# Kernel optimization log

Measured on AMD Instinct MI355X. Metric: run time of the kernel, lower is better.

Reference implementation:

```python
import jax, jax.numpy as jnp
import numpy as np

N_USER, N_FOOD, N_ING, N_CAT, N_HAB = 50000, 50000, 50000, 5000, 5000
N_NODES = N_USER + N_FOOD + N_ING + N_CAT + N_HAB  # 160000
E = 600000
R = 8
D = 128  # common_dim == hidden_dim


def _linear(x, W, b):
    # W: (in, out)
    return x @ W + b


def _rgcn_conv(x, src, dst, edge_type, W, root, bias):
    """PyG RGCNConv with aggr='mean': out = x@root + bias + sum_r mean_{r-edges into i}(W_r x_j)."""
    n = x.shape[0]
    out = x @ root + bias
    for r in range(R):  # static small loop over relations
        mask = (edge_type == r)
        h_r = x @ W[r]                          # (N, O)
        msg = h_r[src] * mask[:, None].astype(x.dtype)  # (E, O)
        s = jax.ops.segment_sum(msg, dst, num_segments=n)
        cnt = jax.ops.segment_sum(mask.astype(x.dtype), dst, num_segments=n)
        out = out + s / jnp.maximum(cnt, 1.0)[:, None]
    return out


def setup_inputs() -> dict:
    key = jax.random.key(0)
    ks = jax.random.split(key, 32)
    s = 0.05
    inp = {
        'x_user': jax.random.normal(ks[0], (N_USER, 256), jnp.float32),
        'x_food': jax.random.normal(ks[1], (N_FOOD, 128), jnp.float32),
        'x_ingredient': jax.random.normal(ks[2], (N_ING, 128), jnp.float32),
        'x_category': jax.random.normal(ks[3], (N_CAT, 64), jnp.float32),
        'x_habit': jax.random.normal(ks[4], (N_HAB, 64), jnp.float32),
        'edge_index': jax.random.randint(ks[5], (2, E), 0, N_NODES, jnp.int32),
        'edge_type': jax.random.randint(ks[6], (E,), 0, R, jnp.int32),
        # init linears (in, out)
        'Wu': jax.random.normal(ks[7], (256, D), jnp.float32) * s,
        'bu': jnp.zeros((D,), jnp.float32),
        'Wf': jax.random.normal(ks[8], (128, D), jnp.float32) * s,
        'bf': jnp.zeros((D,), jnp.float32),
        'Wi': jax.random.normal(ks[9], (128, D), jnp.float32) * s,
        'bi': jnp.zeros((D,), jnp.float32),
        'Wc': jax.random.normal(ks[10], (64, D), jnp.float32) * s,
        'bc': jnp.zeros((D,), jnp.float32),
        'Wh': jax.random.normal(ks[11], (64, D), jnp.float32) * s,
        'bh': jnp.zeros((D,), jnp.float32),
        # conv1
        'W1': jax.random.normal(ks[12], (R, D, D), jnp.float32) * s,
        'root1': jax.random.normal(ks[13], (D, D), jnp.float32) * s,
        'bias1': jnp.zeros((D,), jnp.float32),
        # conv2
        'W2': jax.random.normal(ks[14], (R, D, D), jnp.float32) * s,
        'root2': jax.random.normal(ks[15], (D, D), jnp.float32) * s,
        'bias2': jnp.zeros((D,), jnp.float32),
    }
    return inp


def reference(x_user, x_food, x_ingredient, x_category, x_habit,
              edge_index, edge_type,
              Wu, bu, Wf, bf, Wi, bi, Wc, bc, Wh, bh,
              W1, root1, bias1, W2, root2, bias2):
    # per-type input projections then concat in fixed order
    x_all = jnp.concatenate([
        _linear(x_user, Wu, bu),
        _linear(x_food, Wf, bf),
        _linear(x_ingredient, Wi, bi),
        _linear(x_category, Wc, bc),
        _linear(x_habit, Wh, bh),
    ], axis=0)  # (N_NODES, D)
    src, dst = edge_index[0], edge_index[1]
    x = _rgcn_conv(x_all, src, dst, edge_type, W1, root1, bias1)
    x = jax.nn.relu(x)
    # dropout is identity in eval mode
    x = _rgcn_conv(x, src, dst, edge_type, W2, root2, bias2)
    return x
```

## Files before the change

kernel.cpp:

```cpp
#include <hip/hip_runtime.h>

typedef unsigned short ushort_t;
typedef unsigned int uint_t;
typedef __attribute__((ext_vector_type(8))) __bf16 bf16x8;
typedef __attribute__((ext_vector_type(4))) float f32x4;
typedef __attribute__((ext_vector_type(4))) uint_t uint4v;

#define NN 160000
#define DD 128
#define EE 600000
#define RR 8
#define NRR (NN * RR)
#define WTOT 376832

__device__ __forceinline__ ushort_t f2b(float f) {
  uint_t u = __float_as_uint(f);
  u = u + 0x7fffu + ((u >> 16) & 1u);
  return (ushort_t)(u >> 16);
}
__device__ __forceinline__ float b2f(ushort_t u) {
  return __uint_as_float(((uint_t)u) << 16);
}

struct WSrcs { const float* s[9]; };

__global__ void wconv_all_kernel(WSrcs srcs, ushort_t* __restrict__ wbuf) {
  int i = blockIdx.x * blockDim.x + threadIdx.x;
  if (i >= WTOT) return;
  int m, start, K;
  if      (i < 32768)  { m = 0; start = 0;      K = 256; }
  else if (i < 49152)  { m = 1; start = 32768;  K = 128; }
  else if (i < 65536)  { m = 2; start = 49152;  K = 128; }
  else if (i < 73728)  { m = 3; start = 65536;  K = 64;  }
  else if (i < 81920)  { m = 4; start = 73728;  K = 64;  }
  else if (i < 98304)  { m = 5; start = 81920;  K = 128; }
  else if (i < 114688) { m = 6; start = 98304;  K = 128; }
  else if (i < 245760) { m = 7; start = 114688; K = 128; }
  else                 { m = 8; start = 245760; K = 128; }
  int local = i - start;
  int per = K * 128;
  int mat = local / per, rem = local - mat * per;
  int k = rem >> 7, n = rem & 127;
  wbuf[start + mat * per + n * K + k] = f2b(srcs.s[m][local]);
}

__global__ __launch_bounds__(256, 2) void gemm_proj(
    const float* __restrict__ Ain, const ushort_t* __restrict__ WT,
    const float* __restrict__ bias, ushort_t* __restrict__ Cout, int M, int K) {
  __shared__ ushort_t As[128 * 128];
  __shared__ ushort_t Ws[128 * 128];
  const int tid = threadIdx.x;
  const int bm = blockIdx.x * 128;
  const int wave = tid >> 6, lane = tid & 63;
  const int lr = lane & 15;
  const int lg = lane >> 4;

  f32x4 acc[2][8];
#pragma unroll
  for (int mt = 0; mt < 2; ++mt)
#pragma unroll
    for (int nt = 0; nt < 8; ++nt) acc[mt][nt] = {0.f, 0.f, 0.f, 0.f};

  for (int k0 = 0; k0 < K; k0 += 128) {
#pragma unroll
    for (int it = 0; it < 8; ++it) {
      int row = it * 16 + (tid >> 4);
      int c = tid & 15;
      uint4v val = {0, 0, 0, 0};
      int grow = bm + row, gk = k0 + c * 8;
      if (grow < M && gk < K) {
        const float* ap = Ain + (size_t)grow * K + gk;
        float4 v0 = *(const float4*)ap;
        float4 v1 = *(const float4*)(ap + 4);
        val[0] = (uint_t)f2b(v0.x) | ((uint_t)f2b(v0.y) << 16);
        val[1] = (uint_t)f2b(v0.z) | ((uint_t)f2b(v0.w) << 16);
        val[2] = (uint_t)f2b(v1.x) | ((uint_t)f2b(v1.y) << 16);
        val[3] = (uint_t)f2b(v1.z) | ((uint_t)f2b(v1.w) << 16);
      }
      *(uint4v*)&As[row * 128 + ((c ^ (row & 7)) * 8)] = val;
    }
#pragma unroll
    for (int it = 0; it < 8; ++it) {
      int n = it * 16 + (tid >> 4);
      int c = tid & 15;
      uint4v val = {0, 0, 0, 0};
      int gk = k0 + c * 8;
      if (gk < K)
        val = *(const uint4v*)(WT + (size_t)n * K + gk);
      *(uint4v*)&Ws[n * 128 + ((c ^ (n & 7)) * 8)] = val;
    }
    __syncthreads();
#pragma unroll
    for (int ks = 0; ks < 4; ++ks) {
      int chunk = ks * 4 + lg;
      bf16x8 af[2], bfr[8];
#pragma unroll
      for (int mt = 0; mt < 2; ++mt) {
        int row = wave * 32 + mt * 16 + lr;
        af[mt] = *(const bf16x8*)&As[row * 128 + ((chunk ^ (row & 7)) * 8)];
      }
#pragma unroll
      for (int nt = 0; nt < 8; ++nt) {
        int n = nt * 16 + lr;
        bfr[nt] = *(const bf16x8*)&Ws[n * 128 + ((chunk ^ (n & 7)) * 8)];
      }
#pragma unroll
      for (int mt = 0; mt < 2; ++mt)
#pragma unroll
        for (int nt = 0; nt < 8; ++nt)
          acc[mt][nt] = __builtin_amdgcn_mfma_f32_16x16x32_bf16(
              af[mt], bfr[nt], acc[mt][nt], 0, 0, 0);
    }
    __syncthreads();
  }

  float bv[8];
#pragma unroll
  for (int nt = 0; nt < 8; ++nt) bv[nt] = bias[nt * 16 + lr];

#pragma unroll
  for (int mt = 0; mt < 2; ++mt) {
    int rbase = bm + wave * 32 + mt * 16 + lg * 4;
#pragma unroll
    for (int i = 0; i < 4; ++i) {
      int row = rbase + i;
      if (row >= M) continue;
#pragma unroll
      for (int nt = 0; nt < 8; ++nt)
        Cout[(size_t)row * 128 + nt * 16 + lr] = f2b(acc[mt][nt][i] + bv[nt]);
    }
  }
}

template <bool RELU_BF>
__global__ __launch_bounds__(256, 3) void rgcn_conv(
    const ushort_t* __restrict__ xin, const int* __restrict__ seg_off,
    const int* __restrict__ sorted_src,
    const ushort_t* __restrict__ WrT,
    const ushort_t* __restrict__ rootT,
    const float* __restrict__ bias,
    float* __restrict__ fout, ushort_t* __restrict__ bfout) {
  __shared__ ushort_t As[64 * 128];
  __shared__ ushort_t Ws[128 * 128];
  const int tid = threadIdx.x;
  const int bm = blockIdx.x * 64;
  const int wave = tid >> 6, lane = tid & 63;
  const int lr = lane & 15, lg = lane >> 4;
  const int grp = tid >> 4;
  const int sl = tid & 15;

  f32x4 acc[8];
#pragma unroll
  for (int nt = 0; nt < 8; ++nt) acc[nt] = {0.f, 0.f, 0.f, 0.f};

  for (int ph = 0; ph < 9; ++ph) {
    if (ph == 0) {
#pragma unroll
      for (int q = 0; q < 4; ++q) {
        int row = q * 16 + grp;
        uint4v val = *(const uint4v*)(xin + (size_t)(bm + row) * DD + sl * 8);
        *(uint4v*)&As[row * 128 + ((sl ^ (row & 7)) * 8)] = val;
      }
    } else {
      const int rel = ph - 1;
      int gs[4], ge[4];
#pragma unroll
      for (int q = 0; q < 4; ++q) {
        const int* sp = seg_off + (size_t)rel * NN + (bm + q * 16 + grp);
        gs[q] = sp[0];
        ge[q] = sp[1];
      }
      int fs[4];
#pragma unroll
      for (int q = 0; q < 4; ++q)
        fs[q] = (ge[q] > gs[q]) ? sorted_src[gs[q]] : 0;
      uint4v fv[4];
#pragma unroll
      for (int q = 0; q < 4; ++q)
        fv[q] = *(const uint4v*)(xin + (size_t)fs[q] * DD + sl * 8);

#pragma unroll
      for (int q = 0; q < 4; ++q) {
        int row = q * 16 + grp;
        int cnt = ge[q] - gs[q];
        uint4v o = {0, 0, 0, 0};
        if (cnt == 1) {
          o = fv[q];
        } else if (cnt > 1) {
          float a[8];
#pragma unroll
          for (int j = 0; j < 4; ++j) {
            a[j * 2]     = b2f((ushort_t)(fv[q][j] & 0xffff));
            a[j * 2 + 1] = b2f((ushort_t)(fv[q][j] >> 16));
          }
          for (int i = gs[q] + 1; i < ge[q]; ++i) {
            int s = sorted_src[i];
            uint4v v2 = *(const uint4v*)(xin + (size_t)s * DD + sl * 8);
#pragma unroll
            for (int j = 0; j < 4; ++j) {
              a[j * 2]     += b2f((ushort_t)(v2[j] & 0xffff));
              a[j * 2 + 1] += b2f((ushort_t)(v2[j] >> 16));
            }
          }
          float sc = 1.0f / (float)cnt;
#pragma unroll
          for (int j = 0; j < 4; ++j)
            o[j] = (uint_t)f2b(a[j * 2] * sc) | ((uint_t)f2b(a[j * 2 + 1] * sc) << 16);
        }
        *(uint4v*)&As[row * 128 + ((sl ^ (row & 7)) * 8)] = o;
      }
    }
    const ushort_t* WT = (ph == 0) ? rootT : (WrT + (size_t)(ph - 1) * 16384);
#pragma unroll
    for (int it = 0; it < 8; ++it) {
      int n = it * 16 + grp;
      uint4v val = *(const uint4v*)(WT + (size_t)n * 128 + sl * 8);
      *(uint4v*)&Ws[n * 128 + ((sl ^ (n & 7)) * 8)] = val;
    }
    __syncthreads();

#pragma unroll
    for (int ks = 0; ks < 4; ++ks) {
      int chunk = ks * 4 + lg;
      int arow = wave * 16 + lr;
      bf16x8 af = *(const bf16x8*)&As[arow * 128 + ((chunk ^ (arow & 7)) * 8)];
      bf16x8 bfr[8];
#pragma unroll
      for (int nt = 0; nt < 8; ++nt) {
        int n = nt * 16 + lr;
        bfr[nt] = *(const bf16x8*)&Ws[n * 128 + ((chunk ^ (n & 7)) * 8)];
      }
#pragma unroll
      for (int nt = 0; nt < 8; ++nt)
        acc[nt] = __builtin_amdgcn_mfma_f32_16x16x32_bf16(af, bfr[nt], acc[nt], 0, 0, 0);
    }
    __syncthreads();
  }

  float bv[8];
#pragma unroll
  for (int nt = 0; nt < 8; ++nt) bv[nt] = bias[nt * 16 + lr];

  int rbase = bm + wave * 16 + lg * 4;
#pragma unroll
  for (int i = 0; i < 4; ++i) {
    int row = rbase + i;
#pragma unroll
    for (int nt = 0; nt < 8; ++nt) {
      float v = acc[nt][i] + bv[nt];
      if (RELU_BF)
        bfout[(size_t)row * 128 + nt * 16 + lr] = f2b(fmaxf(v, 0.f));
      else
        fout[(size_t)row * 128 + nt * 16 + lr] = v;
    }
  }
}

__global__ void count_kernel(const int* __restrict__ dstv, const int* __restrict__ et,
                             int* __restrict__ cnt, int E) {
  int e = blockIdx.x * blockDim.x + threadIdx.x;
  if (e < E) atomicAdd(&cnt[(size_t)et[e] * NN + dstv[e]], 1);
}

__global__ __launch_bounds__(256) void scan1_kernel(const int* __restrict__ in, int* __restrict__ out,
                                                    int* __restrict__ partials, int n) {
  __shared__ int sums[256];
  int tid = threadIdx.x;
  int base = blockIdx.x * 2048 + tid * 8;
  int v[8];
  int s = 0;
#pragma unroll
  for (int i = 0; i < 8; ++i) {
    int idx = base + i;
    int x = (idx < n) ? in[idx] : 0;
    v[i] = s;
    s += x;
  }
  sums[tid] = s;
  __syncthreads();
  for (int off = 1; off < 256; off <<= 1) {
    int t = (tid >= off) ? sums[tid - off] : 0;
    __syncthreads();
    sums[tid] += t;
    __syncthreads();
  }
  int excl = (tid == 0) ? 0 : sums[tid - 1];
  if (tid == 255) partials[blockIdx.x] = sums[255];
#pragma unroll
  for (int i = 0; i < 8; ++i) {
    int idx = base + i;
    if (idx < n) out[idx] = excl + v[i];
  }
}

__global__ __launch_bounds__(256) void scan2_kernel(int* __restrict__ partials, int nb) {
  __shared__ int sums[256];
  int tid = threadIdx.x;
  int per = (nb + 255) / 256;
  int start = tid * per;
  int s = 0;
  for (int i = 0; i < per; ++i) {
    int idx = start + i;
    if (idx < nb) s += partials[idx];
  }
  sums[tid] = s;
  __syncthreads();
  for (int off = 1; off < 256; off <<= 1) {
    int t = (tid >= off) ? sums[tid - off] : 0;
    __syncthreads();
    sums[tid] += t;
    __syncthreads();
  }
  int excl = (tid == 0) ? 0 : sums[tid - 1];
  for (int i = 0; i < per; ++i) {
    int idx = start + i;
    if (idx < nb) {
      int t = partials[idx];
      partials[idx] = excl;
      excl += t;
    }
  }
}

__global__ void scan3_kernel(int* __restrict__ out, const int* __restrict__ partials, int n) {
  int base = blockIdx.x * 2048 + threadIdx.x * 8;
  int add = partials[blockIdx.x];
#pragma unroll
  for (int i = 0; i < 8; ++i) {
    int idx = base + i;
    if (idx < n) out[idx] += add;
  }
}

__global__ void sentinel_kernel(int* __restrict__ seg_off) {
  seg_off[NRR] = EE;
}

__global__ void place_kernel(const int* __restrict__ srcv, const int* __restrict__ dstv,
                             const int* __restrict__ et, const int* __restrict__ seg_off,
                             int* __restrict__ cursor, int* __restrict__ sorted_src, int E) {
  int e = blockIdx.x * blockDim.x + threadIdx.x;
  if (e < E) {
    int p = et[e] * NN + dstv[e];
    int slot = seg_off[p] + atomicAdd(&cursor[p], 1);
    sorted_src[slot] = srcv[e];
  }
}

static inline void launch_proj(const float* A, const ushort_t* WT, const float* bias,
                               ushort_t* C, int M, int K, hipStream_t stream) {
  hipLaunchKernelGGL(gemm_proj, dim3((M + 127) / 128), dim3(256), 0, stream,
                     A, WT, bias, C, M, K);
}

extern "C" void kernel_launch(void* const* d_in, const int* in_sizes, int n_in,
                              void* d_out, int out_size, void* d_ws, size_t ws_size,
                              hipStream_t stream) {
  const float* x_user = (const float*)d_in[0];
  const float* x_food = (const float*)d_in[1];
  const float* x_ing  = (const float*)d_in[2];
  const float* x_cat  = (const float*)d_in[3];
  const float* x_hab  = (const float*)d_in[4];
  const int*   eidx   = (const int*)d_in[5];
  const int*   etype  = (const int*)d_in[6];
  const float* Wu = (const float*)d_in[7];
  const float* bu = (const float*)d_in[8];
  const float* Wf = (const float*)d_in[9];
  const float* bfp = (const float*)d_in[10];
  const float* Wi = (const float*)d_in[11];
  const float* bi = (const float*)d_in[12];
  const float* Wc = (const float*)d_in[13];
  const float* bc = (const float*)d_in[14];
  const float* Wh = (const float*)d_in[15];
  const float* bh = (const float*)d_in[16];
  const float* W1    = (const float*)d_in[17];
  const float* root1 = (const float*)d_in[18];
  const float* bias1 = (const float*)d_in[19];
  const float* W2    = (const float*)d_in[20];
  const float* root2 = (const float*)d_in[21];
  const float* bias2 = (const float*)d_in[22];

  const int* src = eidx;
  const int* dst = eidx + EE;

  char* ws = (char*)d_ws;
  ushort_t* xb   = (ushort_t*)(ws);
  ushort_t* xb2  = (ushort_t*)(ws + 40960000);
  int* seg_off   = (int*)(ws + 81920000);
  int* cnt_i     = (int*)(ws + 87040064);
  int* sorted_src= (int*)(ws + 92160064);
  int* pA        = (int*)(ws + 94560064);
  ushort_t* wbuf = (ushort_t*)(ws + 94564160);

  ushort_t* WuT = wbuf;
  ushort_t* WfT = wbuf + 32768;
  ushort_t* WiT = wbuf + 49152;
  ushort_t* WcT = wbuf + 65536;
  ushort_t* WhT = wbuf + 73728;
  ushort_t* r1T = wbuf + 81920;
  ushort_t* r2T = wbuf + 98304;
  ushort_t* W1T = wbuf + 114688;
  ushort_t* W2T = wbuf + 245760;

  float* out = (float*)d_out;

  WSrcs wsrc;
  wsrc.s[0] = Wu; wsrc.s[1] = Wf; wsrc.s[2] = Wi; wsrc.s[3] = Wc; wsrc.s[4] = Wh;
  wsrc.s[5] = root1; wsrc.s[6] = root2; wsrc.s[7] = W1; wsrc.s[8] = W2;
  hipLaunchKernelGGL(wconv_all_kernel, dim3((WTOT + 255) / 256), dim3(256), 0, stream,
                     wsrc, wbuf);

  launch_proj(x_user, WuT, bu, xb + (size_t)0 * DD,      50000, 256, stream);
  launch_proj(x_food, WfT, bfp, xb + (size_t)50000 * DD, 50000, 128, stream);
  launch_proj(x_ing,  WiT, bi, xb + (size_t)100000 * DD, 50000, 128, stream);
  launch_proj(x_cat,  WcT, bc, xb + (size_t)150000 * DD, 5000,  64,  stream);
  launch_proj(x_hab,  WhT, bh, xb + (size_t)155000 * DD, 5000,  64,  stream);

  hipMemsetAsync(cnt_i, 0, (size_t)NRR * 4, stream);
  hipLaunchKernelGGL(count_kernel, dim3((EE + 255) / 256), dim3(256), 0, stream,
                     dst, etype, cnt_i, EE);
  {
    int nb = (NRR + 2047) / 2048;
    hipLaunchKernelGGL(scan1_kernel, dim3(nb), dim3(256), 0, stream, cnt_i, seg_off, pA, NRR);
    hipLaunchKernelGGL(scan2_kernel, dim3(1), dim3(256), 0, stream, pA, nb);
    hipLaunchKernelGGL(scan3_kernel, dim3(nb), dim3(256), 0, stream, seg_off, pA, NRR);
  }
  hipLaunchKernelGGL(sentinel_kernel, dim3(1), dim3(1), 0, stream, seg_off);
  hipMemsetAsync(cnt_i, 0, (size_t)NRR * 4, stream);
  hipLaunchKernelGGL(place_kernel, dim3((EE + 255) / 256), dim3(256), 0, stream,
                     src, dst, etype, seg_off, cnt_i, sorted_src, EE);

  const dim3 convGrid(NN / 64);

  hipLaunchKernelGGL((rgcn_conv<true>), convGrid, dim3(256), 0, stream,
                     xb, seg_off, sorted_src, W1T, r1T, bias1, (float*)nullptr, xb2);

  hipLaunchKernelGGL((rgcn_conv<false>), convGrid, dim3(256), 0, stream,
                     xb2, seg_off, sorted_src, W2T, r2T, bias2, out, (ushort_t*)nullptr);
}
```

Before: 479.5 us.

## Software-pipeline RGCN conv kernel: prefetch neighbor gathers and async-load pre-swizzled weights

Restructures the fused RGCN conv kernel into a multi-stage software pipeline. Segment bounds, source indices and the first two neighbor rows for upcoming relations are fetched several phases ahead. Relation weights are pre-swizzled during weight conversion so they can be copied straight into LDS with global_load_lds while the MFMA loop runs. The root term moves to the final phase, and count-2 neighborhoods get a dedicated path. The aim is to hide gather and weight-load latency behind compute, at the cost of much higher register pressure from large prefetch arrays, which may lower occupancy or cause spills.

```diff
diff --git a/kernel.cpp b/kernel.cpp
--- a/kernel.cpp
+++ b/kernel.cpp
@@ -20,6 +20,12 @@
 }
 __device__ __forceinline__ float b2f(ushort_t u) {
   return __uint_as_float(((uint_t)u) << 16);
+}
+
+__device__ __forceinline__ void gload_lds16(const ushort_t* g, ushort_t* l) {
+  __builtin_amdgcn_global_load_lds(
+      (const __attribute__((address_space(1))) void*)g,
+      (__attribute__((address_space(3))) void*)l, 16, 0, 0);
 }
 
 struct WSrcs { const float* s[9]; };
@@ -41,7 +47,14 @@
   int per = K * 128;
   int mat = local / per, rem = local - mat * per;
   int k = rem >> 7, n = rem & 127;
-  wbuf[start + mat * per + n * K + k] = f2b(srcs.s[m][local]);
+  ushort_t v = f2b(srcs.s[m][local]);
+  if (m < 5) {
+    wbuf[start + mat * per + n * K + k] = v;
+  } else {
+    int kc = k >> 3, kr = k & 7;
+    int slot = kc ^ (n & 7);
+    wbuf[start + mat * per + n * 128 + slot * 8 + kr] = v;
+  }
 }
 
 __global__ __launch_bounds__(256, 2) void gemm_proj(
@@ -153,71 +166,106 @@
 #pragma unroll
   for (int nt = 0; nt < 8; ++nt) acc[nt] = {0.f, 0.f, 0.f, 0.f};
 
-  for (int ph = 0; ph < 9; ++ph) {
-    if (ph == 0) {
-#pragma unroll
-      for (int q = 0; q < 4; ++q) {
-        int row = q * 16 + grp;
-        uint4v val = *(const uint4v*)(xin + (size_t)(bm + row) * DD + sl * 8);
-        *(uint4v*)&As[row * 128 + ((sl ^ (row & 7)) * 8)] = val;
+  int gsv[8][4], gev[8][4];
+  int s0v[8][4], s1v[8][4];
+  uint4v f0v[8][4], f1v[8][4];
+  uint4v rootv[4];
+
+#define BOUNDS(P)                                                         \
+  {                                                                       \
+    _Pragma("unroll") for (int q = 0; q < 4; ++q) {                       \
+      int g = (P) * NN + bm + q * 16 + grp;                               \
+      gsv[P][q] = seg_off[g];                                             \
+      gev[P][q] = seg_off[g + 1];                                         \
+    }                                                                     \
+  }
+
+#define SRCS(P)                                                           \
+  {                                                                       \
+    _Pragma("unroll") for (int q = 0; q < 4; ++q) {                       \
+      int a = gsv[P][q];                                                  \
+      int c = gev[P][q] - a;                                              \
+      int i0 = (a < EE - 1) ? a : (EE - 1);                               \
+      int i1 = (c > 1) ? (a + 1) : i0;                                    \
+      s0v[P][q] = sorted_src[i0];                                         \
+      s1v[P][q] = sorted_src[i1];                                         \
+    }                                                                     \
+  }
+
+#define FVLOAD(P)                                                         \
+  {                                                                       \
+    _Pragma("unroll") for (int q = 0; q < 4; ++q) {                       \
+      f0v[P][q] = *(const uint4v*)(xin + (size_t)s0v[P][q] * DD + sl * 8);\
+      f1v[P][q] = *(const uint4v*)(xin + (size_t)s1v[P][q] * DD + sl * 8);\
+    }                                                                     \
+  }
+
+#define GLLW(SRC)                                                         \
+  {                                                                       \
+    const ushort_t* wsrc = (SRC) + (size_t)wave * 4096 + lane * 8;        \
+    _Pragma("unroll") for (int i = 0; i < 8; ++i)                         \
+      gload_lds16(wsrc + i * 512, &Ws[wave * 4096 + i * 512]);            \
+  }
+
+  BOUNDS(0); BOUNDS(1); BOUNDS(2);
+  GLLW(WrT);
+  SRCS(0); SRCS(1);
+  FVLOAD(0);
+  __builtin_amdgcn_sched_barrier(0);
+
+#pragma unroll
+  for (int p = 0; p < 8; ++p) {
+#pragma unroll
+    for (int q = 0; q < 4; ++q) {
+      int row = q * 16 + grp;
+      int a = gsv[p][q];
+      int c = gev[p][q] - a;
+      uint4v o = {0, 0, 0, 0};
+      if (c == 1) {
+        o = f0v[p][q];
+      } else if (c == 2) {
+        uint4v x0 = f0v[p][q], x1 = f1v[p][q];
+#pragma unroll
+        for (int j = 0; j < 4; ++j) {
+          float e0 = (b2f((ushort_t)(x0[j] & 0xffff)) + b2f((ushort_t)(x1[j] & 0xffff))) * 0.5f;
+          float e1 = (b2f((ushort_t)(x0[j] >> 16)) + b2f((ushort_t)(x1[j] >> 16))) * 0.5f;
+          o[j] = (uint_t)f2b(e0) | ((uint_t)f2b(e1) << 16);
+        }
+      } else if (c >= 3) {
+        uint4v x0 = f0v[p][q], x1 = f1v[p][q];
+        float av[8];
+#pragma unroll
+        for (int j = 0; j < 4; ++j) {
+          av[j * 2]     = b2f((ushort_t)(x0[j] & 0xffff)) + b2f((ushort_t)(x1[j] & 0xffff));
+          av[j * 2 + 1] = b2f((ushort_t)(x0[j] >> 16)) + b2f((ushort_t)(x1[j] >> 16));
+        }
+        for (int i = a + 2; i < a + c; ++i) {
+          int s = sorted_src[i];
+          uint4v v2 = *(const uint4v*)(xin + (size_t)s * DD + sl * 8);
+#pragma unroll
+          for (int j = 0; j < 4; ++j) {
+            av[j * 2]     += b2f((ushort_t)(v2[j] & 0xffff));
+            av[j * 2 + 1] += b2f((ushort_t)(v2[j] >> 16));
+          }
+        }
+        float sc = 1.0f / (float)c;
+#pragma unroll
+        for (int j = 0; j < 4; ++j)
+          o[j] = (uint_t)f2b(av[j * 2] * sc) | ((uint_t)f2b(av[j * 2 + 1] * sc) << 16);
       }
+      *(uint4v*)&As[row * 128 + ((sl ^ (row & 7)) * 8)] = o;
+    }
+
+    __syncthreads();
+
+    if (p < 7) {
+      FVLOAD(p + 1);
     } else {
-      const int rel = ph - 1;
-      int gs[4], ge[4];
-#pragma unroll
-      for (int q = 0; q < 4; ++q) {
-        const int* sp = seg_off + (size_t)rel * NN + (bm + q * 16 + grp);
-        gs[q] = sp[0];
-        ge[q] = sp[1];
-      }
-      int fs[4];
 #pragma unroll
       for (int q = 0; q < 4; ++q)
-        fs[q] = (ge[q] > gs[q]) ? sorted_src[gs[q]] : 0;
-      uint4v fv[4];
-#pragma unroll
-      for (int q = 0; q < 4; ++q)
-        fv[q] = *(const uint4v*)(xin + (size_t)fs[q] * DD + sl * 8);
-
-#pragma unroll
-      for (int q = 0; q < 4; ++q) {
-        int row = q * 16 + grp;
-        int cnt = ge[q] - gs[q];
-        uint4v o = {0, 0, 0, 0};
-        if (cnt == 1) {
-          o = fv[q];
-        } else if (cnt > 1) {
-          float a[8];
-#pragma unroll
-          for (int j = 0; j < 4; ++j) {
-            a[j * 2]     = b2f((ushort_t)(fv[q][j] & 0xffff));
-            a[j * 2 + 1] = b2f((ushort_t)(fv[q][j] >> 16));
-          }
-          for (int i = gs[q] + 1; i < ge[q]; ++i) {
-            int s = sorted_src[i];
-            uint4v v2 = *(const uint4v*)(xin + (size_t)s * DD + sl * 8);
-#pragma unroll
-            for (int j = 0; j < 4; ++j) {
-              a[j * 2]     += b2f((ushort_t)(v2[j] & 0xffff));
-              a[j * 2 + 1] += b2f((ushort_t)(v2[j] >> 16));
-            }
-          }
-          float sc = 1.0f / (float)cnt;
-#pragma unroll
-          for (int j = 0; j < 4; ++j)
-            o[j] = (uint_t)f2b(a[j * 2] * sc) | ((uint_t)f2b(a[j * 2 + 1] * sc) << 16);
-        }
-        *(uint4v*)&As[row * 128 + ((sl ^ (row & 7)) * 8)] = o;
-      }
-    }
-    const ushort_t* WT = (ph == 0) ? rootT : (WrT + (size_t)(ph - 1) * 16384);
-#pragma unroll
-    for (int it = 0; it < 8; ++it) {
-      int n = it * 16 + grp;
-      uint4v val = *(const uint4v*)(WT + (size_t)n * 128 + sl * 8);
-      *(uint4v*)&Ws[n * 128 + ((sl ^ (n & 7)) * 8)] = val;
-    }
-    __syncthreads();
+        rootv[q] = *(const uint4v*)(xin + (size_t)(bm + q * 16 + grp) * DD + sl * 8);
+    }
+    __builtin_amdgcn_sched_barrier(0);
 
 #pragma unroll
     for (int ks = 0; ks < 4; ++ks) {
@@ -234,7 +282,41 @@
       for (int nt = 0; nt < 8; ++nt)
         acc[nt] = __builtin_amdgcn_mfma_f32_16x16x32_bf16(af, bfr[nt], acc[nt], 0, 0, 0);
     }
-    __syncthreads();
+
+    asm volatile("s_waitcnt lgkmcnt(0)" ::: "memory");
+    __builtin_amdgcn_s_barrier();
+    __builtin_amdgcn_sched_barrier(0);
+
+    if (p < 7) {
+      GLLW(WrT + (size_t)(p + 1) * 16384);
+    } else {
+      GLLW(rootT);
+    }
+    if (p < 6) { SRCS(p + 2); }
+    if (p < 5) { BOUNDS(p + 3); }
+    __builtin_amdgcn_sched_barrier(0);
+  }
+
+#pragma unroll
+  for (int q = 0; q < 4; ++q) {
+    int row = q * 16 + grp;
+    *(uint4v*)&As[row * 128 + ((sl ^ (row & 7)) * 8)] = rootv[q];
+  }
+  __syncthreads();
+#pragma unroll
+  for (int ks = 0; ks < 4; ++ks) {
+    int chunk = ks * 4 + lg;
+    int arow = wave * 16 + lr;
+    bf16x8 af = *(const bf16x8*)&As[arow * 128 + ((chunk ^ (arow & 7)) * 8)];
+    bf16x8 bfr[8];
+#pragma unroll
+    for (int nt = 0; nt < 8; ++nt) {
+      int n = nt * 16 + lr;
+      bfr[nt] = *(const bf16x8*)&Ws[n * 128 + ((chunk ^ (n & 7)) * 8)];
+    }
+#pragma unroll
+    for (int nt = 0; nt < 8; ++nt)
+      acc[nt] = __builtin_amdgcn_mfma_f32_16x16x32_bf16(af, bfr[nt], acc[nt], 0, 0, 0);
   }
 
   float bv[8];
@@ -254,6 +336,10 @@
         fout[(size_t)row * 128 + nt * 16 + lr] = v;
     }
   }
+#undef BOUNDS
+#undef SRCS
+#undef FVLOAD
+#undef GLLW
 }
 
 __global__ void count_kernel(const int* __restrict__ dstv, const int* __restrict__ et,
```

Result: faster. 385.9 us (-19.5%).

## Restructure RGCN conv: register-resident aggregates, LDS-resident weight halves, 1024-thread blocks

Applied to the files above, without the earlier changes.

The conv kernel now uses 1024-thread blocks over 256 rows. It splits K into two 64-wide halves and loads all nine weight slabs for each half into LDS at once via global_load_lds, using a new pre-swizzled weight image. Gathered neighbour means are built directly in registers as MFMA A-operands, with a software pipeline that prefetches segment bounds, source indices and features for upcoming relations. This removes the per-relation As staging and the barriers between phases. In exchange, neighbours are gathered twice (once per K half), register pressure is higher, and the sentinel kernel is folded into scan3.

```diff
diff --git a/kernel.cpp b/kernel.cpp
--- a/kernel.cpp
+++ b/kernel.cpp
@@ -12,6 +12,7 @@
 #define RR 8
 #define NRR (NN * RR)
 #define WTOT 376832
+#define HALF_ELEMS 73728
 
 __device__ __forceinline__ ushort_t f2b(float f) {
   uint_t u = __float_as_uint(f);
@@ -20,6 +21,12 @@
 }
 __device__ __forceinline__ float b2f(ushort_t u) {
   return __uint_as_float(((uint_t)u) << 16);
+}
+
+__device__ __forceinline__ void gload_lds16(const ushort_t* g, ushort_t* l) {
+  __builtin_amdgcn_global_load_lds(
+      (const __attribute__((address_space(1))) void*)g,
+      (__attribute__((address_space(3))) void*)l, 16, 0, 0);
 }
 
 struct WSrcs { const float* s[9]; };
@@ -41,7 +48,18 @@
   int per = K * 128;
   int mat = local / per, rem = local - mat * per;
   int k = rem >> 7, n = rem & 127;
-  wbuf[start + mat * per + n * K + k] = f2b(srcs.s[m][local]);
+  ushort_t v = f2b(srcs.s[m][local]);
+  if (m < 5) {
+    wbuf[start + mat * per + n * K + k] = v;
+    return;
+  }
+  int conv = (m == 5 || m == 7) ? 0 : 1;
+  int slab = (m <= 6) ? 8 : mat;
+  int kh = k >> 6, kl = k & 63;
+  int kc = kl >> 3, kr = kl & 7;
+  size_t off = 81920 + (size_t)conv * 2 * HALF_ELEMS + (size_t)kh * HALF_ELEMS
+             + (size_t)slab * 8192 + n * 64 + ((kc ^ (n & 7)) * 8 + kr);
+  wbuf[off] = v;
 }
 
 __global__ __launch_bounds__(256, 2) void gemm_proj(
@@ -133,108 +151,151 @@
 }
 
 template <bool RELU_BF>
-__global__ __launch_bounds__(256, 3) void rgcn_conv(
+__global__ __launch_bounds__(1024, 4) void rgcn_conv(
     const ushort_t* __restrict__ xin, const int* __restrict__ seg_off,
     const int* __restrict__ sorted_src,
-    const ushort_t* __restrict__ WrT,
-    const ushort_t* __restrict__ rootT,
+    const ushort_t* __restrict__ wimg,
     const float* __restrict__ bias,
     float* __restrict__ fout, ushort_t* __restrict__ bfout) {
-  __shared__ ushort_t As[64 * 128];
-  __shared__ ushort_t Ws[128 * 128];
+  __shared__ ushort_t Ws[HALF_ELEMS];
   const int tid = threadIdx.x;
-  const int bm = blockIdx.x * 64;
   const int wave = tid >> 6, lane = tid & 63;
   const int lr = lane & 15, lg = lane >> 4;
-  const int grp = tid >> 4;
-  const int sl = tid & 15;
+  const int bm = blockIdx.x * 256;
+  const int d = bm + wave * 16 + lr;
 
   f32x4 acc[8];
 #pragma unroll
   for (int nt = 0; nt < 8; ++nt) acc[nt] = {0.f, 0.f, 0.f, 0.f};
 
-  for (int ph = 0; ph < 9; ++ph) {
-    if (ph == 0) {
-#pragma unroll
-      for (int q = 0; q < 4; ++q) {
-        int row = q * 16 + grp;
-        uint4v val = *(const uint4v*)(xin + (size_t)(bm + row) * DD + sl * 8);
-        *(uint4v*)&As[row * 128 + ((sl ^ (row & 7)) * 8)] = val;
-      }
-    } else {
-      const int rel = ph - 1;
-      int gs[4], ge[4];
-#pragma unroll
-      for (int q = 0; q < 4; ++q) {
-        const int* sp = seg_off + (size_t)rel * NN + (bm + q * 16 + grp);
-        gs[q] = sp[0];
-        ge[q] = sp[1];
-      }
-      int fs[4];
-#pragma unroll
-      for (int q = 0; q < 4; ++q)
-        fs[q] = (ge[q] > gs[q]) ? sorted_src[gs[q]] : 0;
-      uint4v fv[4];
-#pragma unroll
-      for (int q = 0; q < 4; ++q)
-        fv[q] = *(const uint4v*)(xin + (size_t)fs[q] * DD + sl * 8);
-
-#pragma unroll
-      for (int q = 0; q < 4; ++q) {
-        int row = q * 16 + grp;
-        int cnt = ge[q] - gs[q];
-        uint4v o = {0, 0, 0, 0};
-        if (cnt == 1) {
-          o = fv[q];
-        } else if (cnt > 1) {
-          float a[8];
+#define GLOADW(SRC)                                                       \
+  {                                                                       \
+    const ushort_t* wsrc = (SRC) + (size_t)wave * 4608 + lane * 8;        \
+    _Pragma("unroll") for (int i = 0; i < 9; ++i)                         \
+      gload_lds16(wsrc + i * 512, &Ws[wave * 4608 + i * 512]);            \
+  }
+
+#pragma unroll
+  for (int kh = 0; kh < 2; ++kh) {
+    const int kb = kh * 64;
+
+    if (kh == 1) __builtin_amdgcn_s_barrier();
+    GLOADW(wimg + (size_t)kh * HALF_ELEMS);
+    asm volatile("s_waitcnt vmcnt(0)" ::: "memory");
+    __builtin_amdgcn_s_barrier();
+
+    int a_[9], c_[9], s0_[9], s1_[9];
+    uint4v f00[9], f01[9], f10[9], f11[9];
+
+#define BOUNDS(P)                                                         \
+  {                                                                       \
+    int g = (P) * NN + d;                                                 \
+    a_[P] = seg_off[g];                                                   \
+    c_[P] = seg_off[g + 1] - a_[P];                                       \
+  }
+
+#define SRCS(P)                                                           \
+  {                                                                       \
+    int a = a_[P], c = c_[P];                                             \
+    int i0 = (a < EE - 1) ? a : (EE - 1);                                 \
+    int i1 = (c > 1) ? (a + 1) : i0;                                      \
+    s0_[P] = sorted_src[i0];                                              \
+    s1_[P] = sorted_src[i1];                                              \
+  }
+
+#define FVLOAD(P)                                                         \
+  {                                                                       \
+    if (c_[P] > 0) {                                                      \
+      const ushort_t* rp = xin + (size_t)s0_[P] * DD + kb + lg * 8;       \
+      f00[P] = *(const uint4v*)rp;                                        \
+      f01[P] = *(const uint4v*)(rp + 32);                                 \
+    }                                                                     \
+    if (c_[P] > 1) {                                                      \
+      const ushort_t* rp = xin + (size_t)s1_[P] * DD + kb + lg * 8;       \
+      f10[P] = *(const uint4v*)rp;                                        \
+      f11[P] = *(const uint4v*)(rp + 32);                                 \
+    }                                                                     \
+  }
+
+    BOUNDS(0); BOUNDS(1); BOUNDS(2);
+    SRCS(0); SRCS(1);
+    FVLOAD(0);
+    uint4v r0v, r1v;
+
+#pragma unroll
+    for (int p = 0; p < 9; ++p) {
+      if (p < 7) { FVLOAD(p + 1); }
+      else if (p == 7) {
+        const ushort_t* rp = xin + (size_t)d * DD + kb + lg * 8;
+        r0v = *(const uint4v*)rp;
+        r1v = *(const uint4v*)(rp + 32);
+      }
+      if (p + 2 < 8) { SRCS(p + 2); }
+      if (p + 3 < 8) { BOUNDS(p + 3); }
+
+      uint4v o0 = {0, 0, 0, 0}, o1 = {0, 0, 0, 0};
+      if (p == 8) {
+        o0 = r0v; o1 = r1v;
+      } else {
+        int a = a_[p], c = c_[p];
+        if (c == 1) {
+          o0 = f00[p]; o1 = f01[p];
+        } else if (c == 2) {
 #pragma unroll
           for (int j = 0; j < 4; ++j) {
-            a[j * 2]     = b2f((ushort_t)(fv[q][j] & 0xffff));
-            a[j * 2 + 1] = b2f((ushort_t)(fv[q][j] >> 16));
+            float e0 = (b2f((ushort_t)(f00[p][j] & 0xffff)) + b2f((ushort_t)(f10[p][j] & 0xffff))) * 0.5f;
+            float e1 = (b2f((ushort_t)(f00[p][j] >> 16)) + b2f((ushort_t)(f10[p][j] >> 16))) * 0.5f;
+            o0[j] = (uint_t)f2b(e0) | ((uint_t)f2b(e1) << 16);
+            float g0 = (b2f((ushort_t)(f01[p][j] & 0xffff)) + b2f((ushort_t)(f11[p][j] & 0xffff))) * 0.5f;
+            float g1 = (b2f((ushort_t)(f01[p][j] >> 16)) + b2f((ushort_t)(f11[p][j] >> 16))) * 0.5f;
+            o1[j] = (uint_t)f2b(g0) | ((uint_t)f2b(g1) << 16);
           }
-          for (int i = gs[q] + 1; i < ge[q]; ++i) {
+        } else if (c >= 3) {
+          float av[8], bw[8];
+#pragma unroll
+          for (int j = 0; j < 4; ++j) {
+            av[j * 2]     = b2f((ushort_t)(f00[p][j] & 0xffff)) + b2f((ushort_t)(f10[p][j] & 0xffff));
+            av[j * 2 + 1] = b2f((ushort_t)(f00[p][j] >> 16)) + b2f((ushort_t)(f10[p][j] >> 16));
+            bw[j * 2]     = b2f((ushort_t)(f01[p][j] & 0xffff)) + b2f((ushort_t)(f11[p][j] & 0xffff));
+            bw[j * 2 + 1] = b2f((ushort_t)(f01[p][j] >> 16)) + b2f((ushort_t)(f11[p][j] >> 16));
+          }
+          for (int i = a + 2; i < a + c; ++i) {
             int s = sorted_src[i];
-            uint4v v2 = *(const uint4v*)(xin + (size_t)s * DD + sl * 8);
+            const ushort_t* rp = xin + (size_t)s * DD + kb + lg * 8;
+            uint4v x0 = *(const uint4v*)rp;
+            uint4v x1 = *(const uint4v*)(rp + 32);
 #pragma unroll
             for (int j = 0; j < 4; ++j) {
-              a[j * 2]     += b2f((ushort_t)(v2[j] & 0xffff));
-              a[j * 2 + 1] += b2f((ushort_t)(v2[j] >> 16));
+              av[j * 2]     += b2f((ushort_t)(x0[j] & 0xffff));
+              av[j * 2 + 1] += b2f((ushort_t)(x0[j] >> 16));
+              bw[j * 2]     += b2f((ushort_t)(x1[j] & 0xffff));
+              bw[j * 2 + 1] += b2f((ushort_t)(x1[j] >> 16));
             }
           }
-          float sc = 1.0f / (float)cnt;
-#pragma unroll
-          for (int j = 0; j < 4; ++j)
-            o[j] = (uint_t)f2b(a[j * 2] * sc) | ((uint_t)f2b(a[j * 2 + 1] * sc) << 16);
+          float sc = 1.0f / (float)c;
+#pragma unroll
+          for (int j = 0; j < 4; ++j) {
+            o0[j] = (uint_t)f2b(av[j * 2] * sc) | ((uint_t)f2b(av[j * 2 + 1] * sc) << 16);
+            o1[j] = (uint_t)f2b(bw[j * 2] * sc) | ((uint_t)f2b(bw[j * 2 + 1] * sc) << 16);
+          }
         }
-        *(uint4v*)&As[row * 128 + ((sl ^ (row & 7)) * 8)] = o;
-      }
-    }
-    const ushort_t* WT = (ph == 0) ? rootT : (WrT + (size_t)(ph - 1) * 16384);
-#pragma unroll
-    for (int it = 0; it < 8; ++it) {
-      int n = it * 16 + grp;
-      uint4v val = *(const uint4v*)(WT + (size_t)n * 128 + sl * 8);
-      *(uint4v*)&Ws[n * 128 + ((sl ^ (n & 7)) * 8)] = val;
-    }
-    __syncthreads();
-
-#pragma unroll
-    for (int ks = 0; ks < 4; ++ks) {
-      int chunk = ks * 4 + lg;
-      int arow = wave * 16 + lr;
-      bf16x8 af = *(const bf16x8*)&As[arow * 128 + ((chunk ^ (arow & 7)) * 8)];
-      bf16x8 bfr[8];
+      }
+      bf16x8 af0 = *(bf16x8*)&o0;
+      bf16x8 af1 = *(bf16x8*)&o1;
+
+      const int rb = p * 8192;
 #pragma unroll
       for (int nt = 0; nt < 8; ++nt) {
         int n = nt * 16 + lr;
-        bfr[nt] = *(const bf16x8*)&Ws[n * 128 + ((chunk ^ (n & 7)) * 8)];
-      }
-#pragma unroll
-      for (int nt = 0; nt < 8; ++nt)
-        acc[nt] = __builtin_amdgcn_mfma_f32_16x16x32_bf16(af, bfr[nt], acc[nt], 0, 0, 0);
-    }
-    __syncthreads();
+        bf16x8 w0 = *(const bf16x8*)&Ws[rb + n * 64 + ((lg ^ (n & 7)) * 8)];
+        bf16x8 w1 = *(const bf16x8*)&Ws[rb + n * 64 + (((4 + lg) ^ (n & 7)) * 8)];
+        acc[nt] = __builtin_amdgcn_mfma_f32_16x16x32_bf16(af0, w0, acc[nt], 0, 0, 0);
+        acc[nt] = __builtin_amdgcn_mfma_f32_16x16x32_bf16(af1, w1, acc[nt], 0, 0, 0);
+      }
+    }
+#undef BOUNDS
+#undef SRCS
+#undef FVLOAD
   }
 
   float bv[8];
@@ -254,6 +315,7 @@
         fout[(size_t)row * 128 + nt * 16 + lr] = v;
     }
   }
+#undef GLOADW
 }
 
 __global__ void count_kernel(const int* __restrict__ dstv, const int* __restrict__ et,
@@ -330,10 +392,7 @@
     int idx = base + i;
     if (idx < n) out[idx] += add;
   }
-}
-
-__global__ void sentinel_kernel(int* __restrict__ seg_off) {
-  seg_off[NRR] = EE;
+  if (blockIdx.x == 0 && threadIdx.x == 0) out[n] = EE;
 }
 
 __global__ void place_kernel(const int* __restrict__ srcv, const int* __restrict__ dstv,
@@ -397,10 +456,8 @@
   ushort_t* WiT = wbuf + 49152;
   ushort_t* WcT = wbuf + 65536;
   ushort_t* WhT = wbuf + 73728;
-  ushort_t* r1T = wbuf + 81920;
-  ushort_t* r2T = wbuf + 98304;
-  ushort_t* W1T = wbuf + 114688;
-  ushort_t* W2T = wbuf + 245760;
+  ushort_t* img1 = wbuf + 81920;
+  ushort_t* img2 = wbuf + 81920 + 2 * HALF_ELEMS;
 
   float* out = (float*)d_out;
 
@@ -425,16 +482,15 @@
     hipLaunchKernelGGL(scan2_kernel, dim3(1), dim3(256), 0, stream, pA, nb);
     hipLaunchKernelGGL(scan3_kernel, dim3(nb), dim3(256), 0, stream, seg_off, pA, NRR);
   }
-  hipLaunchKernelGGL(sentinel_kernel, dim3(1), dim3(1), 0, stream, seg_off);
   hipMemsetAsync(cnt_i, 0, (size_t)NRR * 4, stream);
   hipLaunchKernelGGL(place_kernel, dim3((EE + 255) / 256), dim3(256), 0, stream,
                      src, dst, etype, seg_off, cnt_i, sorted_src, EE);
 
-  const dim3 convGrid(NN / 64);
-
-  hipLaunchKernelGGL((rgcn_conv<true>), convGrid, dim3(256), 0, stream,
-                     xb, seg_off, sorted_src, W1T, r1T, bias1, (float*)nullptr, xb2);
-
-  hipLaunchKernelGGL((rgcn_conv<false>), convGrid, dim3(256), 0, stream,
-                     xb2, seg_off, sorted_src, W2T, r2T, bias2, out, (ushort_t*)nullptr);
-}
+  const dim3 convGrid(NN / 256);
+
+  hipLaunchKernelGGL((rgcn_conv<true>), convGrid, dim3(1024), 0, stream,
+                     xb, seg_off, sorted_src, img1, bias1, (float*)nullptr, xb2);
+
+  hipLaunchKernelGGL((rgcn_conv<false>), convGrid, dim3(1024), 0, stream,
+                     xb2, seg_off, sorted_src, img2, bias2, out, (ushort_t*)nullptr);
+}
```

Measured after the change: 918.7 us. +91.6%, slower.
